# Optimization experiments

Hardware: AMD Instinct MI355X
Metric: run time of the kernel (lower is better)

## Reference

```python
import jax, jax.numpy as jnp
import numpy as np

# (dv=3, dc=6)-regular Tanner graph: M checks, N=2M vars, E=M*dc edges
M, N, DV, DC, D, B, T = 1024, 2048, 3, 6, 8, 128, 5
CIN = DC * D          # check-MLP in/out dim = 48
VIN = DV * D + 1      # var-MLP in/out dim  = 25 (extra scalar = LLR)
HC, HV = 4 * CIN, 4 * VIN
EPS = 1e-6


def _graph():
    # variable j connects to checks (j + l) % M, l = 0..DV-1 -> every check has degree DC
    var_nbrs = (np.arange(N)[:, None] + np.arange(DV)[None, :]) % M   # [N, DV] check ids
    # var-edge id e = j*DV + l ; sort edges by check to get check-slot ordering
    order = np.argsort(var_nbrs.reshape(-1), kind='stable')           # check-edge p -> var-edge e
    chk_nbrs = (order // DV).reshape(M, DC)                           # var id in each check slot
    inv_order = np.argsort(order)                                     # var-edge e -> check-edge p
    return chk_nbrs, order, inv_order


def setup_inputs() -> dict:
    key = jax.random.key(0)
    ks = jax.random.split(key, 12)
    chk_nbrs, order, inv_order = _graph()
    prior = np.clip(np.random.default_rng(0).uniform(0.005, 0.05, size=N), EPS, 1 - EPS)
    prior_llr = jnp.asarray(np.log((1.0 - prior) / prior), jnp.float32)

    def lin_w(k, g, nin, nout):
        return jax.random.normal(k, (g, nin, nout), jnp.float32) / np.sqrt(nin)

    def lin_b(k, g, nout):
        return 0.02 * jax.random.normal(k, (g, nout), jnp.float32)

    return {
        "syndromes": jax.random.randint(ks[0], (B, M), 0, 2, jnp.int32),
        "prior_llr": prior_llr,
        "chk_w1": lin_w(ks[1], M, CIN, HC), "chk_b1": lin_b(ks[2], M, HC),
        "chk_w2": lin_w(ks[3], M, HC, CIN), "chk_b2": lin_b(ks[4], M, CIN),
        "var_w1": lin_w(ks[5], N, VIN, HV), "var_b1": lin_b(ks[6], N, HV),
        "var_w2": lin_w(ks[7], N, HV, VIN), "var_b2": lin_b(ks[8], N, VIN),
        "chk_nbrs": jnp.asarray(chk_nbrs, jnp.int32),      # [M, DC] var id per check slot
        "c2v_gather": jnp.asarray(inv_order, jnp.int32),   # var-edge -> check-edge perm
        "v2c_gather": jnp.asarray(order, jnp.int32),       # check-edge -> var-edge perm
    }


def reference(syndromes, prior_llr, chk_w1, chk_b1, chk_w2, chk_b2,
              var_w1, var_b1, var_w2, var_b2, chk_nbrs, c2v_gather, v2c_gather):
    synd_sgn = (1 - 2 * syndromes).astype(jnp.float32)                    # [B, M]
    prior_b = jnp.broadcast_to(prior_llr, (B, N))[..., None]              # [B, N, 1]

    def chk_mlp(x):  # x: [B, M, CIN], per-check grouped GEMM
        h = jax.nn.gelu(jnp.einsum('bmi,mih->bmh', x, chk_w1) + chk_b1, approximate=False)
        return jnp.einsum('bmh,mho->bmo', h, chk_w2) + chk_b2

    def var_mlp(x):  # x: [B, N, VIN]
        h = jax.nn.gelu(jnp.einsum('bni,nih->bnh', x, var_w1) + var_b1, approximate=False)
        return jnp.einsum('bnh,nho->bno', h, var_w2) + var_b2

    # init check in-messages: zeros with first component = prior LLR of neighbor var
    chk_in = jnp.zeros((B, M, DC, D), jnp.float32).at[..., 0].set(prior_llr[chk_nbrs][None])

    def step(chk_in, _):
        y = chk_mlp(chk_in.reshape(B, M, CIN)).reshape(B, M, DC, D)
        y = y * synd_sgn[:, :, None, None]                                # syndrome sign flip
        var_in = y.reshape(B, M * DC, D)[:, c2v_gather]                   # scatter c->v as gather
        x = jnp.concatenate([var_in.reshape(B, N, DV * D), prior_b], axis=-1)
        out = var_mlp(x)
        llr = out[..., DV * D]                                            # [B, N]
        msg = out[..., :DV * D].reshape(B, N * DV, D)
        chk_in_new = msg[:, v2c_gather].reshape(B, M, DC, D)              # scatter v->c as gather
        return chk_in_new, llr

    _, llrs = jax.lax.scan(step, chk_in, None, length=T)
    return llrs  # [T, B, N]
```

## Files before the change

kernel.cpp:

```cpp
#include <hip/hip_runtime.h>
#include <math.h>

#define MM 1024
#define NN 2048
#define BB 128
#define TT 5
#define EE 6144

typedef __bf16 bf16x8 __attribute__((ext_vector_type(8)));
typedef __bf16 bf16x4 __attribute__((ext_vector_type(4)));
typedef short  s16x4  __attribute__((ext_vector_type(4)));
typedef float  f32x4  __attribute__((ext_vector_type(4)));
typedef unsigned int u32x4 __attribute__((ext_vector_type(4)));

#define CHK_W_ELEMS 22272
#define CHK_L2_OFF  12288
#define VAR_W_ELEMS 7168
#define VAR_L2_OFF  3584

__device__ __forceinline__ float gelu_fast(float x) {
    float xe = x * 0.70710678118654752f;
    float ax = fabsf(xe);
    float t  = __builtin_amdgcn_rcpf(1.0f + 0.3275911f * ax);
    float p  = t * (0.254829592f + t * (-0.284496736f + t * (1.421413741f +
               t * (-1.453152027f + t * 1.061405429f))));
    float er = 1.0f - p * __expf(-xe * xe);
    er = copysignf(er, xe);
    return 0.5f * x * (1.0f + er);
}

__device__ __forceinline__ f32x4 mfma16(bf16x4 a, bf16x4 b, f32x4 c) {
#if __has_builtin(__builtin_amdgcn_mfma_f32_16x16x16bf16_1k)
    return __builtin_amdgcn_mfma_f32_16x16x16bf16_1k(
        __builtin_bit_cast(s16x4, a), __builtin_bit_cast(s16x4, b), c, 0, 0, 0);
#else
    f32x4 d;
    asm volatile("v_mfma_f32_16x16x16_bf16 %0, %1, %2, %3\n\ts_nop 4"
                 : "=v"(d) : "v"(a), "v"(b), "v"(c));
    return d;
#endif
}

__device__ __forceinline__ void wave_lds_fence() {
    asm volatile("s_waitcnt lgkmcnt(0)" ::: "memory");
}

#define PREP_GRID (1024 + 2048 + 512 + 3072)

__global__ __launch_bounds__(256, 6)
void prep_fused(const float* __restrict__ cw1, const float* __restrict__ cb1,
                const float* __restrict__ cw2, const float* __restrict__ cb2,
                const float* __restrict__ vw1, const float* __restrict__ vb1,
                const float* __restrict__ vw2, const float* __restrict__ vb2,
                const int* __restrict__ synd, const float* __restrict__ prior,
                __bf16* __restrict__ wchk, __bf16* __restrict__ wvar,
                float* __restrict__ sgnT, __bf16* __restrict__ v2c)
{
    const int bid = blockIdx.x;
    const int tid = threadIdx.x;
    const int w = tid >> 6, l = tid & 63, q = l >> 4, c = l & 15;

    __shared__ __align__(16) float s[6656];
    float* sw = s + w * 1664;

    if (bid < 1024) {
        const int m = bid;
        const float* w1p = cw1 + (size_t)m * 9216;
        const float* w2p = cw2 + (size_t)m * 9216;
        __bf16* dst = wchk + (size_t)m * CHK_W_ELEMS;

        #pragma unroll
        for (int i0 = 0; i0 < 6; ++i0) {
            int i = i0 * 64 + l;
            int r = i / 12, c4 = i % 12;
            float4 v = *(const float4*)(w1p + r * 192 + w * 48 + c4 * 4);
            *(float2*)(sw + r * 50 + c4 * 4)     = make_float2(v.x, v.y);
            *(float2*)(sw + r * 50 + c4 * 4 + 2) = make_float2(v.z, v.w);
        }
        wave_lds_fence();
        #pragma unroll
        for (int d = 0; d < 3; ++d) {
            int mt = 3 * w + d;
            bf16x8 v;
            #pragma unroll
            for (int j = 0; j < 8; ++j)
                v[j] = (__bf16)sw[(q * 8 + j) * 50 + d * 16 + c];
            *(bf16x8*)(dst + (mt * 2) * 512 + l * 8) = v;
        }
        wave_lds_fence();

        #pragma unroll
        for (int i0 = 0; i0 < 4; ++i0) {
            int i = i0 * 64 + l;
            if (i < 204) {
                int r = i / 12, c4 = i % 12;
                const float* src = (r < 16)
                    ? (w1p + (32 + r) * 192 + w * 48 + c4 * 4)
                    : (cb1 + (size_t)m * 192 + w * 48 + c4 * 4);
                float4 v = *(const float4*)src;
                *(float2*)(sw + r * 50 + c4 * 4)     = make_float2(v.x, v.y);
                *(float2*)(sw + r * 50 + c4 * 4 + 2) = make_float2(v.z, v.w);
            }
        }
        wave_lds_fence();
        #pragma unroll
        for (int d = 0; d < 3; ++d) {
            int mt = 3 * w + d;
            bf16x8 v;
            #pragma unroll
            for (int j = 0; j < 8; ++j) {
                int lr = q * 8 + j;
                float wv = sw[lr * 50 + d * 16 + c];
                v[j] = (__bf16)((lr <= 16) ? wv : 0.0f);
            }
            *(bf16x8*)(dst + (mt * 2 + 1) * 512 + l * 8) = v;
        }
        wave_lds_fence();

        for (int t = w; t < 10; t += 4) {
            if (t < 9) {
                const int kb = t / 3, mt = t - kb * 3;
                #pragma unroll
                for (int i0 = 0; i0 < 4; ++i0) {
                    int i = i0 * 64 + l;
                    int r = i >> 2, c4 = i & 3;
                    float4 v = *(const float4*)(w2p + (kb * 64 + r) * 48 + mt * 16 + c4 * 4);
                    *(float4*)(sw + r * 20 + c4 * 4) = v;
                }
                wave_lds_fence();
                #pragma unroll
                for (int kk = 0; kk < 4; ++kk) {
                    bf16x4 v;
                    #pragma unroll
                    for (int r = 0; r < 4; ++r)
                        v[r] = (__bf16)sw[(kk * 16 + q * 4 + r) * 20 + c];
                    *(bf16x4*)(dst + CHK_L2_OFF + ((kb * 4 + kk) * 3 + mt) * 256 + l * 4) = v;
                }
                wave_lds_fence();
            } else {
                #pragma unroll
                for (int mt = 0; mt < 3; ++mt) {
                    bf16x4 v;
                    #pragma unroll
                    for (int r = 0; r < 4; ++r) v[r] = (__bf16)0.0f;
                    if (q == 0) v[0] = (__bf16)cb2[(size_t)m * 48 + mt * 16 + c];
                    *(bf16x4*)(dst + CHK_L2_OFF + (36 + mt) * 256 + l * 4) = v;
                }
            }
        }
    } else if (bid < 3072) {
        const int nv = bid - 1024;
        const float* w1p = vw1 + (size_t)nv * 2500;
        const float* w2p = vw2 + (size_t)nv * 2500;
        __bf16* dst = wvar + (size_t)nv * VAR_W_ELEMS;

        if (w < 3) {
            #pragma unroll
            for (int i0 = 0; i0 < 4; ++i0) {
                int i = i0 * 64 + l;
                if (i < 208) {
                    int r = i >> 3, c4 = i & 7;
                    const float* src = (r < 25)
                        ? (w1p + r * 100 + w * 32 + c4 * 4)
                        : (vb1 + (size_t)nv * 100 + w * 32 + c4 * 4);
                    float4 v = *(const float4*)src;
                    *(float2*)(sw + r * 34 + c4 * 4)     = make_float2(v.x, v.y);
                    *(float2*)(sw + r * 34 + c4 * 4 + 2) = make_float2(v.z, v.w);
                }
            }
        } else {
            if (l < 26) {
                int r = l;
                const float* src = (r < 25) ? (w1p + r * 100 + 96)
                                            : (vb1 + (size_t)nv * 100 + 96);
                float4 v = *(const float4*)src;
                *(float2*)(sw + r * 34)     = make_float2(v.x, v.y);
                *(float2*)(sw + r * 34 + 2) = make_float2(v.z, v.w);
            }
        }
        wave_lds_fence();
        {
            const int nmt = (w < 3) ? 2 : 1;
            #pragma unroll
            for (int d = 0; d < 2; ++d) {
                if (d < nmt) {
                    const int mt = (w < 3) ? (2 * w + d) : 6;
                    const int h = mt * 16 + c;
                    bf16x8 v;
                    #pragma unroll
                    for (int j = 0; j < 8; ++j) {
                        int k = q * 8 + j;
                        float wv = sw[k * 34 + d * 16 + c];
                        v[j] = (__bf16)((h < 100 && k <= 25) ? wv : 0.0f);
                    }
                    *(bf16x8*)(dst + mt * 512 + l * 8) = v;
                }
            }
        }
        wave_lds_fence();

        if (w < 3) {
            #pragma unroll
            for (int i0 = 0; i0 < 4; ++i0) {
                int i = i0 * 64 + l;
                if (i < 200)
                    *(float4*)(sw + i * 4) = *(const float4*)(w2p + 800 * w + i * 4);
            }
        } else {
            if (l < 25) *(float4*)(sw + l * 4) = *(const float4*)(w2p + 2400 + l * 4);
            if (l < 25) sw[100 + l] = vb2[(size_t)nv * 25 + l];
        }
        wave_lds_fence();
        {
            const int nks = (w < 3) ? 2 : 1;
            #pragma unroll
            for (int kk = 0; kk < 2; ++kk) {
                if (kk < nks) {
                    const int ks = (w < 3) ? (2 * w + kk) : 6;
                    #pragma unroll
                    for (int mt = 0; mt < 2; ++mt) {
                        const int o = mt * 16 + c;
                        bf16x4 v;
                        #pragma unroll
                        for (int r = 0; r < 4; ++r) {
                            float x;
                            if (w < 3) {
                                int lk = kk * 16 + q * 4 + r;
                                float wv = sw[lk * 25 + o];
                                x = (o < 25) ? wv : 0.0f;
                            } else {
                                int lk = q * 4 + r;
                                float wv = sw[lk * 25 + o];
                                x = (o < 25 && lk <= 4) ? wv : 0.0f;
                            }
                            v[r] = (__bf16)x;
                        }
                        *(bf16x4*)(dst + VAR_L2_OFF + (ks * 2 + mt) * 256 + l * 4) = v;
                    }
                }
            }
        }
    } else if (bid < 3584) {
        int idx = (bid - 3072) * 256 + tid;
        int m = idx >> 7, b = idx & 127;
        sgnT[idx] = (float)(1 - 2 * synd[(size_t)b * MM + m]);
    } else {
        int idx = (bid - 3584) * 256 + tid;
        int e = idx >> 7;
        bf16x8 v;
        #pragma unroll
        for (int j = 0; j < 8; ++j) v[j] = (__bf16)0.0f;
        v[0] = (__bf16)prior[e / 3];
        *(bf16x8*)(v2c + (size_t)idx * 8) = v;
    }
}

#define CPITCH 58
__global__ __launch_bounds__(256, 3)
void chk_kernel(const __bf16* __restrict__ wchk,
                const float* __restrict__ sgnT,
                const int* __restrict__ v2c_gather,
                const __bf16* __restrict__ v2c, __bf16* __restrict__ c2v)
{
    const int m = blockIdx.x;
    const int tid = threadIdx.x;
    const int w = tid >> 6, l = tid & 63, q = l >> 4, c = l & 15;

    __shared__ __align__(16) __bf16 wlds[CHK_W_ELEMS];
    __shared__ __align__(16) __bf16 ytile[4 * 16 * CPITCH];
    {
        const __bf16* src = wchk + (size_t)m * CHK_W_ELEMS;
        for (int i = tid; i < CHK_W_ELEMS / 8; i += 256)
            *(u32x4*)(wlds + i * 8) = *(const u32x4*)(src + i * 8);
    }
    const int e0 = v2c_gather[m * 6 + q];
    const int e1 = (q < 2) ? v2c_gather[m * 6 + 4 + q] : 0;
    __syncthreads();

    __bf16* myy = ytile + w * 16 * CPITCH;

    for (int t2 = 0; t2 < 2; ++t2) {
        const int bt = t2 * 64 + w * 16;

        bf16x8 b0 = *(const bf16x8*)(v2c + ((size_t)e0 * BB + bt + c) * 8);
        bf16x8 b1f;
        #pragma unroll
        for (int j = 0; j < 8; ++j) b1f[j] = (__bf16)0.0f;
        if (q < 2)       b1f = *(const bf16x8*)(v2c + ((size_t)e1 * BB + bt + c) * 8);
        else if (q == 2) b1f[0] = (__bf16)1.0f;

        f32x4 acc[12];
        #pragma unroll
        for (int mt = 0; mt < 12; ++mt) {
            bf16x8 a0 = *(const bf16x8*)(wlds + (mt * 2 + 0) * 512 + l * 8);
            bf16x8 a1 = *(const bf16x8*)(wlds + (mt * 2 + 1) * 512 + l * 8);
            f32x4 z = {0.f, 0.f, 0.f, 0.f};
            z = __builtin_amdgcn_mfma_f32_16x16x32_bf16(a0, b0, z, 0, 0, 0);
            z = __builtin_amdgcn_mfma_f32_16x16x32_bf16(a1, b1f, z, 0, 0, 0);
            acc[mt] = z;
        }

        f32x4 acc2[3];
        #pragma unroll
        for (int mt = 0; mt < 3; ++mt) acc2[mt] = (f32x4){0.f, 0.f, 0.f, 0.f};
        #pragma unroll
        for (int ks = 0; ks < 13; ++ks) {
            bf16x4 bf;
            if (ks < 12) {
                #pragma unroll
                for (int r = 0; r < 4; ++r) bf[r] = (__bf16)gelu_fast(acc[ks][r]);
            } else {
                #pragma unroll
                for (int r = 0; r < 4; ++r) bf[r] = (__bf16)0.0f;
                if (q == 0) bf[0] = (__bf16)1.0f;
            }
            #pragma unroll
            for (int mt = 0; mt < 3; ++mt) {
                bf16x4 af = *(const bf16x4*)(wlds + CHK_L2_OFF + (ks * 3 + mt) * 256 + l * 4);
                acc2[mt] = mfma16(af, bf, acc2[mt]);
            }
        }

        const float sg = sgnT[m * BB + bt + c];
        #pragma unroll
        for (int mt = 0; mt < 3; ++mt)
            #pragma unroll
            for (int r = 0; r < 4; ++r)
                myy[c * CPITCH + mt * 16 + q * 4 + r] = (__bf16)(acc2[mt][r] * sg);
        wave_lds_fence();

        {
            int s = l >> 4, row = l & 15;
            u32x4 vv = *(const u32x4*)(myy + row * CPITCH + s * 8);
            *(u32x4*)(c2v + ((size_t)(m * 6 + s) * BB + bt + row) * 8) = vv;
            if (l < 32) {
                int s2 = 4 + (l >> 4), row2 = l & 15;
                u32x4 v2 = *(const u32x4*)(myy + row2 * CPITCH + s2 * 8);
                *(u32x4*)(c2v + ((size_t)(m * 6 + s2) * BB + bt + row2) * 8) = v2;
            }
        }
        wave_lds_fence();
    }
}

#define VPITCH 26
__global__ __launch_bounds__(256, 4)
void var_kernel(const __bf16* __restrict__ wvar,
                const int* __restrict__ c2v_gather, const float* __restrict__ prior,
                const __bf16* __restrict__ c2v, __bf16* __restrict__ v2c,
                float* __restrict__ llr_out, int last)
{
    const int nv = blockIdx.x;
    const int tid = threadIdx.x;
    const int w = tid >> 6, l = tid & 63, q = l >> 4, c = l & 15;

    __shared__ __align__(16) __bf16 wlds[VAR_W_ELEMS];
    __shared__ __align__(16) __bf16 ytile[4 * 16 * VPITCH];
    {
        const __bf16* src = wvar + (size_t)nv * VAR_W_ELEMS;
        for (int i = tid; i < VAR_W_ELEMS / 8; i += 256)
            *(u32x4*)(wlds + i * 8) = *(const u32x4*)(src + i * 8);
    }
    const int ep = (q < 3) ? c2v_gather[nv * 3 + q] : 0;
    const __bf16 prbf = (__bf16)prior[nv];
    __syncthreads();

    __bf16* myy = ytile + w * 16 * VPITCH;

    for (int t2 = 0; t2 < 2; ++t2) {
        const int bt = t2 * 64 + w * 16;

        bf16x8 b0;
        #pragma unroll
        for (int j = 0; j < 8; ++j) b0[j] = (__bf16)0.0f;
        if (q < 3) b0 = *(const bf16x8*)(c2v + ((size_t)ep * BB + bt + c) * 8);
        else { b0[0] = prbf; b0[1] = (__bf16)1.0f; }

        f32x4 acc[7];
        #pragma unroll
        for (int mt = 0; mt < 7; ++mt) {
            bf16x8 a0 = *(const bf16x8*)(wlds + mt * 512 + l * 8);
            f32x4 z = {0.f, 0.f, 0.f, 0.f};
            acc[mt] = __builtin_amdgcn_mfma_f32_16x16x32_bf16(a0, b0, z, 0, 0, 0);
        }

        f32x4 acc2[2];
        acc2[0] = (f32x4){0.f, 0.f, 0.f, 0.f};
        acc2[1] = (f32x4){0.f, 0.f, 0.f, 0.f};
        #pragma unroll
        for (int ks = 0; ks < 7; ++ks) {
            bf16x4 bf;
            #pragma unroll
            for (int r = 0; r < 4; ++r) bf[r] = (__bf16)gelu_fast(acc[ks][r]);
            if (ks == 6 && q == 1) bf[0] = (__bf16)1.0f;
            #pragma unroll
            for (int mt = 0; mt < 2; ++mt) {
                bf16x4 af = *(const bf16x4*)(wlds + VAR_L2_OFF + (ks * 2 + mt) * 256 + l * 4);
                acc2[mt] = mfma16(af, bf, acc2[mt]);
            }
        }

        #pragma unroll
        for (int r = 0; r < 4; ++r)
            myy[c * VPITCH + q * 4 + r] = (__bf16)acc2[0][r];
        if (q < 2)
            #pragma unroll
            for (int r = 0; r < 4; ++r)
                myy[c * VPITCH + 16 + q * 4 + r] = (__bf16)acc2[1][r];
        if (q == 2) llr_out[(size_t)(bt + c) * NN + nv] = acc2[1][0];
        wave_lds_fence();

        if (!last && l < 48) {
            int s = l >> 4, row = l & 15;
            u32x4 vv = *(const u32x4*)(myy + row * VPITCH + s * 8);
            *(u32x4*)(v2c + ((size_t)(nv * 3 + s) * BB + bt + row) * 8) = vv;
        }
        wave_lds_fence();
    }
}

extern "C" void kernel_launch(void* const* d_in, const int* in_sizes, int n_in,
                              void* d_out, int out_size, void* d_ws, size_t ws_size,
                              hipStream_t stream) {
    const int*   syndromes = (const int*)  d_in[0];
    const float* prior_llr = (const float*)d_in[1];
    const float* chk_w1    = (const float*)d_in[2];
    const float* chk_b1    = (const float*)d_in[3];
    const float* chk_w2    = (const float*)d_in[4];
    const float* chk_b2    = (const float*)d_in[5];
    const float* var_w1    = (const float*)d_in[6];
    const float* var_b1    = (const float*)d_in[7];
    const float* var_w2    = (const float*)d_in[8];
    const float* var_b2    = (const float*)d_in[9];
    const int*   c2v_g     = (const int*)  d_in[11];
    const int*   v2c_g     = (const int*)  d_in[12];

    float* out = (float*)d_out;

    __bf16* v2c  = (__bf16*)d_ws;
    __bf16* c2v  = v2c + (size_t)EE * BB * 8;
    __bf16* wchk = c2v + (size_t)EE * BB * 8;
    __bf16* wvar = wchk + (size_t)MM * CHK_W_ELEMS;
    float*  sgnT = (float*)(wvar + (size_t)NN * VAR_W_ELEMS);

    prep_fused<<<PREP_GRID, 256, 0, stream>>>(chk_w1, chk_b1, chk_w2, chk_b2,
                                              var_w1, var_b1, var_w2, var_b2,
                                              syndromes, prior_llr,
                                              wchk, wvar, sgnT, v2c);

    for (int t = 0; t < TT; ++t) {
        chk_kernel<<<MM, 256, 0, stream>>>(wchk, sgnT, v2c_g, v2c, c2v);
        var_kernel<<<NN, 256, 0, stream>>>(wvar, c2v_g, prior_llr, c2v, v2c,
                                           out + (size_t)t * BB * NN,
                                           (t == TT - 1) ? 1 : 0);
    }
}
```

Before: 399.3 us.

## Stream MLP weights via direct global-to-LDS loads and overlap with layer-1 compute

```diff
diff --git a/kernel.cpp b/kernel.cpp
--- a/kernel.cpp
+++ b/kernel.cpp
@@ -12,6 +12,9 @@
 typedef short  s16x4  __attribute__((ext_vector_type(4)));
 typedef float  f32x4  __attribute__((ext_vector_type(4)));
 typedef unsigned int u32x4 __attribute__((ext_vector_type(4)));
+
+typedef const __attribute__((address_space(1))) void* gas_p;
+typedef __attribute__((address_space(3))) void* las_p;
 
 #define CHK_W_ELEMS 22272
 #define CHK_L2_OFF  12288
@@ -255,6 +258,44 @@
     }
 }
 
+__device__ __forceinline__ void chk_layer1(const __bf16* wlds, int l,
+                                           bf16x8 b0, bf16x8 b1, f32x4* acc)
+{
+    #pragma unroll
+    for (int mt = 0; mt < 12; ++mt) {
+        bf16x8 a0 = *(const bf16x8*)(wlds + (mt * 2 + 0) * 512 + l * 8);
+        bf16x8 a1 = *(const bf16x8*)(wlds + (mt * 2 + 1) * 512 + l * 8);
+        f32x4 z = {0.f, 0.f, 0.f, 0.f};
+        z = __builtin_amdgcn_mfma_f32_16x16x32_bf16(a0, b0, z, 0, 0, 0);
+        z = __builtin_amdgcn_mfma_f32_16x16x32_bf16(a1, b1, z, 0, 0, 0);
+        acc[mt] = z;
+    }
+}
+
+__device__ __forceinline__ void chk_layer2(const __bf16* wlds, int l, int q,
+                                           const f32x4* acc, f32x4* acc2)
+{
+    #pragma unroll
+    for (int mt = 0; mt < 3; ++mt) acc2[mt] = (f32x4){0.f, 0.f, 0.f, 0.f};
+    #pragma unroll
+    for (int ks = 0; ks < 13; ++ks) {
+        bf16x4 bf;
+        if (ks < 12) {
+            #pragma unroll
+            for (int r = 0; r < 4; ++r) bf[r] = (__bf16)gelu_fast(acc[ks][r]);
+        } else {
+            #pragma unroll
+            for (int r = 0; r < 4; ++r) bf[r] = (__bf16)0.0f;
+            if (q == 0) bf[0] = (__bf16)1.0f;
+        }
+        #pragma unroll
+        for (int mt = 0; mt < 3; ++mt) {
+            bf16x4 af = *(const bf16x4*)(wlds + CHK_L2_OFF + (ks * 3 + mt) * 256 + l * 4);
+            acc2[mt] = mfma16(af, bf, acc2[mt]);
+        }
+    }
+}
+
 #define CPITCH 58
 __global__ __launch_bounds__(256, 3)
 void chk_kernel(const __bf16* __restrict__ wchk,
@@ -268,65 +309,63 @@
 
     __shared__ __align__(16) __bf16 wlds[CHK_W_ELEMS];
     __shared__ __align__(16) __bf16 ytile[4 * 16 * CPITCH];
+
+    const int e0 = v2c_gather[m * 6 + q];
+    const int e1 = (q < 2) ? v2c_gather[m * 6 + 4 + q] : 0;
+
+    bf16x8 bA[2], bB[2];
+    float sg[2];
+    #pragma unroll
+    for (int t2 = 0; t2 < 2; ++t2) {
+        const int bt = t2 * 64 + w * 16;
+        bA[t2] = *(const bf16x8*)(v2c + ((size_t)e0 * BB + bt + c) * 8);
+        bf16x8 bb;
+        #pragma unroll
+        for (int j = 0; j < 8; ++j) bb[j] = (__bf16)0.0f;
+        if (q < 2)       bb = *(const bf16x8*)(v2c + ((size_t)e1 * BB + bt + c) * 8);
+        else if (q == 2) bb[0] = (__bf16)1.0f;
+        bB[t2] = bb;
+        sg[t2] = sgnT[m * BB + bt + c];
+    }
+
     {
         const __bf16* src = wchk + (size_t)m * CHK_W_ELEMS;
-        for (int i = tid; i < CHK_W_ELEMS / 8; i += 256)
-            *(u32x4*)(wlds + i * 8) = *(const u32x4*)(src + i * 8);
-    }
-    const int e0 = v2c_gather[m * 6 + q];
-    const int e1 = (q < 2) ? v2c_gather[m * 6 + 4 + q] : 0;
+        #pragma unroll
+        for (int r = 0; r < 10; ++r)
+            __builtin_amdgcn_global_load_lds(
+                (gas_p)(src + (r * 256 + tid) * 8),
+                (las_p)(wlds + (r * 256 + tid) * 8), 16, 0, 0);
+        if (tid < 224)
+            __builtin_amdgcn_global_load_lds(
+                (gas_p)(src + (2560 + tid) * 8),
+                (las_p)(wlds + (2560 + tid) * 8), 16, 0, 0);
+    }
+    __builtin_amdgcn_sched_barrier(0);
+    asm volatile("s_waitcnt vmcnt(5)" ::: "memory");
     __syncthreads();
 
     __bf16* myy = ytile + w * 16 * CPITCH;
 
+    f32x4 acc[12];
+    chk_layer1(wlds, l, bA[0], bB[0], acc);
+
+    __builtin_amdgcn_sched_barrier(0);
+    asm volatile("s_waitcnt vmcnt(0)" ::: "memory");
+    __syncthreads();
+
+    #pragma unroll
     for (int t2 = 0; t2 < 2; ++t2) {
+        if (t2 == 1) chk_layer1(wlds, l, bA[1], bB[1], acc);
         const int bt = t2 * 64 + w * 16;
 
-        bf16x8 b0 = *(const bf16x8*)(v2c + ((size_t)e0 * BB + bt + c) * 8);
-        bf16x8 b1f;
-        #pragma unroll
-        for (int j = 0; j < 8; ++j) b1f[j] = (__bf16)0.0f;
-        if (q < 2)       b1f = *(const bf16x8*)(v2c + ((size_t)e1 * BB + bt + c) * 8);
-        else if (q == 2) b1f[0] = (__bf16)1.0f;
-
-        f32x4 acc[12];
-        #pragma unroll
-        for (int mt = 0; mt < 12; ++mt) {
-            bf16x8 a0 = *(const bf16x8*)(wlds + (mt * 2 + 0) * 512 + l * 8);
-            bf16x8 a1 = *(const bf16x8*)(wlds + (mt * 2 + 1) * 512 + l * 8);
-            f32x4 z = {0.f, 0.f, 0.f, 0.f};
-            z = __builtin_amdgcn_mfma_f32_16x16x32_bf16(a0, b0, z, 0, 0, 0);
-            z = __builtin_amdgcn_mfma_f32_16x16x32_bf16(a1, b1f, z, 0, 0, 0);
-            acc[mt] = z;
-        }
-
         f32x4 acc2[3];
-        #pragma unroll
-        for (int mt = 0; mt < 3; ++mt) acc2[mt] = (f32x4){0.f, 0.f, 0.f, 0.f};
-        #pragma unroll
-        for (int ks = 0; ks < 13; ++ks) {
-            bf16x4 bf;
-            if (ks < 12) {
-                #pragma unroll
-                for (int r = 0; r < 4; ++r) bf[r] = (__bf16)gelu_fast(acc[ks][r]);
-            } else {
-                #pragma unroll
-                for (int r = 0; r < 4; ++r) bf[r] = (__bf16)0.0f;
-                if (q == 0) bf[0] = (__bf16)1.0f;
-            }
-            #pragma unroll
-            for (int mt = 0; mt < 3; ++mt) {
-                bf16x4 af = *(const bf16x4*)(wlds + CHK_L2_OFF + (ks * 3 + mt) * 256 + l * 4);
-                acc2[mt] = mfma16(af, bf, acc2[mt]);
-            }
-        }
-
-        const float sg = sgnT[m * BB + bt + c];
+        chk_layer2(wlds, l, q, acc, acc2);
+
         #pragma unroll
         for (int mt = 0; mt < 3; ++mt)
             #pragma unroll
             for (int r = 0; r < 4; ++r)
-                myy[c * CPITCH + mt * 16 + q * 4 + r] = (__bf16)(acc2[mt][r] * sg);
+                myy[c * CPITCH + mt * 16 + q * 4 + r] = (__bf16)(acc2[mt][r] * sg[t2]);
         wave_lds_fence();
 
         {
@@ -344,7 +383,7 @@
 }
 
 #define VPITCH 26
-__global__ __launch_bounds__(256, 4)
+__global__ __launch_bounds__(256, 5)
 void var_kernel(const __bf16* __restrict__ wvar,
                 const int* __restrict__ c2v_gather, const float* __restrict__ prior,
                 const __bf16* __restrict__ c2v, __bf16* __restrict__ v2c,
@@ -356,25 +395,44 @@
 
     __shared__ __align__(16) __bf16 wlds[VAR_W_ELEMS];
     __shared__ __align__(16) __bf16 ytile[4 * 16 * VPITCH];
+
+    const int ep = (q < 3) ? c2v_gather[nv * 3 + q] : 0;
+    const __bf16 prbf = (__bf16)prior[nv];
+
+    bf16x8 bp[2];
+    #pragma unroll
+    for (int t2 = 0; t2 < 2; ++t2) {
+        const int bt = t2 * 64 + w * 16;
+        bf16x8 bb;
+        #pragma unroll
+        for (int j = 0; j < 8; ++j) bb[j] = (__bf16)0.0f;
+        if (q < 3) bb = *(const bf16x8*)(c2v + ((size_t)ep * BB + bt + c) * 8);
+        else { bb[0] = prbf; bb[1] = (__bf16)1.0f; }
+        bp[t2] = bb;
+    }
+
     {
         const __bf16* src = wvar + (size_t)nv * VAR_W_ELEMS;
-        for (int i = tid; i < VAR_W_ELEMS / 8; i += 256)
-            *(u32x4*)(wlds + i * 8) = *(const u32x4*)(src + i * 8);
-    }
-    const int ep = (q < 3) ? c2v_gather[nv * 3 + q] : 0;
-    const __bf16 prbf = (__bf16)prior[nv];
+        #pragma unroll
+        for (int r = 0; r < 3; ++r)
+            __builtin_amdgcn_global_load_lds(
+                (gas_p)(src + (r * 256 + tid) * 8),
+                (las_p)(wlds + (r * 256 + tid) * 8), 16, 0, 0);
+        if (tid < 128)
+            __builtin_amdgcn_global_load_lds(
+                (gas_p)(src + (768 + tid) * 8),
+                (las_p)(wlds + (768 + tid) * 8), 16, 0, 0);
+    }
+    __builtin_amdgcn_sched_barrier(0);
+    asm volatile("s_waitcnt vmcnt(0)" ::: "memory");
     __syncthreads();
 
     __bf16* myy = ytile + w * 16 * VPITCH;
 
+    #pragma unroll
     for (int t2 = 0; t2 < 2; ++t2) {
         const int bt = t2 * 64 + w * 16;
-
-        bf16x8 b0;
-        #pragma unroll
-        for (int j = 0; j < 8; ++j) b0[j] = (__bf16)0.0f;
-        if (q < 3) b0 = *(const bf16x8*)(c2v + ((size_t)ep * BB + bt + c) * 8);
-        else { b0[0] = prbf; b0[1] = (__bf16)1.0f; }
+        const bf16x8 b0 = bp[t2];
 
         f32x4 acc[7];
         #pragma unroll
```

New measurement: 386.8 us. 1.03x faster.
